# Kernel optimization log

Measured on AMD Instinct MI355X. Metric: run time of the kernel, lower is better.

Reference implementation:

```python
import jax, jax.numpy as jnp
import numpy as np

NEG = 1e12  # matches the torch code's -1e12 '-inf' substitute


def setup_inputs() -> dict:
    key = jax.random.key(0)
    k1, k2, k3, k4 = jax.random.split(key, 4)
    B, L, H, O = 8, 512, 768, 12
    inputs = jax.random.normal(k1, (B, L, H), dtype=jnp.float32)
    mask = jax.random.randint(k2, (B, L), 0, 2, dtype=jnp.int32)
    # kaiming-uniform-ish init scale
    bound1 = 1.0 / np.sqrt(H)
    weight1 = jax.random.uniform(k3, (H, O, H), dtype=jnp.float32, minval=-bound1, maxval=bound1)
    bound2 = 1.0 / np.sqrt(2 * H + 1)
    weight2 = jax.random.uniform(k4, (2 * H + 1, O), dtype=jnp.float32, minval=-bound2, maxval=bound2)
    return {"inputs": inputs, "weight1": weight1, "weight2": weight2, "mask": mask}


def reference(inputs, weight1, weight2, mask):
    B, L, H = inputs.shape
    # bilinear term: bxyo = x_i W1 x_j
    logits1 = jnp.einsum('bxi,ioj,byj->bxyo', inputs, weight1, inputs)
    # linear term: equivalent to cat([x_i, x_j, 1]) @ weight2, without the O(L^2*H) intermediate.
    # concat_x[b,i,j] = [inputs[b,i], inputs[b,j], 1]
    wa = weight2[:H]          # multiplies x_i (the x2/row side)
    wb = weight2[H:2 * H]     # multiplies x_j (the x1/col side)
    bias = weight2[2 * H]     # multiplies the ones column
    lin_i = inputs @ wa       # [B, L, O]
    lin_j = inputs @ wb       # [B, L, O]
    logits = logits1 + lin_i[:, :, None, :] + lin_j[:, None, :, :] + bias
    logits = jnp.transpose(logits, (0, 3, 1, 2))  # [B, O, L, L]
    m = mask.astype(logits.dtype)
    m_row = m[:, None, :, None]  # mask on axis ndim-2
    m_col = m[:, None, None, :]  # mask on axis ndim-1
    logits = logits * m_row - NEG * (1.0 - m_row)
    logits = logits * m_col - NEG * (1.0 - m_col)
    tril = jnp.tril(jnp.ones((L, L), logits.dtype), k=-1)
    logits = logits - tril * NEG
    return logits
```

## Files before the change

### kernel.cpp

```cpp
#include <hip/hip_runtime.h>


#define NEGV 1e12f

typedef __attribute__((ext_vector_type(4))) float f32x4;
typedef __attribute__((ext_vector_type(8))) int   i32x8;

__device__ __forceinline__ unsigned char f2fp8(float f) {
    union { float f; unsigned u; } c; c.f = f;
    unsigned s = (c.u >> 24) & 0x80;
    unsigned a = c.u & 0x7FFFFFFF;
    if (a < 0x3C800000u) return (unsigned char)s;
    a += 0x80000;
    int e = (int)(a >> 23) - 127;
    unsigned m = (a >> 20) & 7;
    if (e > 8 || (e == 8 && m == 7)) return (unsigned char)(s | 0x7E);
    return (unsigned char)(s | ((e + 7) << 3) | m);
}

__device__ __forceinline__ unsigned pk_fp8x2(float a, float b) {
#if __has_builtin(__builtin_amdgcn_cvt_pk_fp8_f32)
    return (unsigned)__builtin_amdgcn_cvt_pk_fp8_f32(a, b, 0, false) & 0xFFFFu;
#else
    return (unsigned)f2fp8(a) | ((unsigned)f2fp8(b) << 8);
#endif
}

__device__ __forceinline__ float fp8_to_f32(unsigned char b) {
#if __has_builtin(__builtin_amdgcn_cvt_f32_fp8)
    return __builtin_amdgcn_cvt_f32_fp8((int)b, 0);
#else
    const int s = b >> 7, e = (b >> 3) & 15, m = b & 7;
    float mag = e ? __builtin_ldexpf((float)(8 + m), e - 10)
                  : __builtin_ldexpf((float)m, -9);
    return s ? -mag : mag;
#endif
}

__device__ __forceinline__ unsigned f2fp4(float f) {
    const float a = fabsf(f);
    const unsigned s = (__float_as_uint(f) >> 28) & 8u;
    unsigned c;
    if      (a < 0.25f) c = 0;
    else if (a < 0.75f) c = 1;
    else if (a < 1.25f) c = 2;
    else if (a < 1.75f) c = 3;
    else if (a < 2.5f)  c = 4;
    else if (a < 3.5f)  c = 5;
    else if (a < 5.0f)  c = 6;
    else                c = 7;
    return s | c;
}

#define GLDS(gp, lp) __builtin_amdgcn_global_load_lds( \
    (__attribute__((address_space(1))) void*)(gp),     \
    (__attribute__((address_space(3))) void*)(lp), 16, 0, 0)

__global__ __launch_bounds__(256) void prep_kernel(
    const float* __restrict__ in, const float* __restrict__ w1,
    const float* __restrict__ w2, unsigned* __restrict__ A4,
    unsigned* __restrict__ A8, unsigned char* __restrict__ W4) {
    __shared__ float t[64][68];
    const int bx  = blockIdx.x;
    const int tid = threadIdx.x;
    if (bx < 1536) {
        const int i = bx * 256 + tid;
        const float4 v0 = ((const float4*)in)[2 * i];
        const float4 v1 = ((const float4*)in)[2 * i + 1];
        A4[i] = f2fp4(v0.x * 2.0f)        | (f2fp4(v0.y * 2.0f) << 4)
              | (f2fp4(v0.z * 2.0f) << 8) | (f2fp4(v0.w * 2.0f) << 12)
              | (f2fp4(v1.x * 2.0f) << 16)| (f2fp4(v1.y * 2.0f) << 20)
              | (f2fp4(v1.z * 2.0f) << 24)| (f2fp4(v1.w * 2.0f) << 28);
        A8[2 * i]     = pk_fp8x2(v0.x, v0.y) | (pk_fp8x2(v0.z, v0.w) << 16);
        A8[2 * i + 1] = pk_fp8x2(v1.x, v1.y) | (pk_fp8x2(v1.z, v1.w) << 16);
    } else if (bx < 3264) {
        const int b2 = bx - 1536;
        const int n0 = (b2 % 144) * 64;
        const int i0 = (b2 / 144) * 64;
        const int g  = tid >> 4;
        const int q  = tid & 15;
        #pragma unroll
        for (int p = 0; p < 4; ++p) {
            const int il = p * 16 + g;
            float4 v = *(const float4*)(w1 + (size_t)(i0 + il) * 9216 + n0 + q * 4);
            *(float4*)&t[il][q * 4] = v;
        }
        __syncthreads();
        #pragma unroll
        for (int p = 0; p < 2; ++p) {
            const int nl = p * 32 + (tid >> 3);
            const int iq = (tid & 7) * 8;
            unsigned w = 0;
            #pragma unroll
            for (int e = 0; e < 8; ++e)
                w |= f2fp4(t[iq + e][nl] * 128.0f) << (4 * e);
            *(unsigned*)(W4 + (size_t)(n0 + nl) * 384 + (i0 >> 1) + (tid & 7) * 4) = w;
        }
    } else {
        const int j = bx - 3264;
        unsigned char* dst = W4 + (size_t)(9216 + j) * 384;
        if (j < 24) {
            if (tid < 128) {
                const int h0 = tid * 6;
                #pragma unroll
                for (int k = 0; k < 3; ++k) {
                    const int h = h0 + 2 * k;
                    const int c0 = (j < 12) ? (h * 12 + j)       : ((768 + h) * 12 + (j - 12));
                    const int c1 = (j < 12) ? ((h + 1) * 12 + j) : ((769 + h) * 12 + (j - 12));
                    dst[(h >> 1)] = (unsigned char)(f2fp4(w2[c0] * 128.0f)
                                                  | (f2fp4(w2[c1] * 128.0f) << 4));
                }
            }
        } else {
            if (tid < 96) ((unsigned*)dst)[tid] = 0u;
        }
    }
}

__device__ __forceinline__ void gemm256_fp4(
    const unsigned char* __restrict__ A, int lda,
    const unsigned char* __restrict__ B, int ldb,
    char* As, char* Bs, f32x4 (&acc)[8][4], int sA, int sB) {
    const int tid  = threadIdx.x;
    const int lane = tid & 63;
    const int wave = tid >> 6;
    const unsigned char* aSrc[4]; const unsigned char* bSrc[4];
    int off[4];
    #pragma unroll
    for (int p = 0; p < 4; ++p) {
        const int cc = tid + 512 * p;
        const int row = cc >> 3, slot = cc & 7;
        const int g = slot ^ (row & 7);
        aSrc[p] = A + (size_t)row * lda + g * 16;
        bSrc[p] = B + (size_t)row * ldb + g * 16;
        off[p] = cc * 16;
    }
    const int wm = (wave >> 2) * 128;
    const int wn = (wave & 3) * 64;
    const int fr = lane & 15;
    const int kg = lane >> 4;

#define READ_FRAG4(dst, buf, rr, kk) do {                                         \
        const uint4 q_ = *(const uint4*)((buf) + (rr) * 128 +                     \
                                         (((kk) * 4 + kg) ^ ((rr) & 7)) * 16);    \
        dst[0] = q_.x; dst[1] = q_.y; dst[2] = q_.z; dst[3] = q_.w;               \
        dst[4] = 0; dst[5] = 0; dst[6] = 0; dst[7] = 0;                           \
    } while (0)

    #pragma unroll
    for (int p = 0; p < 4; ++p) GLDS(aSrc[p], As + off[p]);
    #pragma unroll
    for (int p = 0; p < 4; ++p) GLDS(bSrc[p], Bs + off[p]);
    __syncthreads();
    int cur = 0;
    #pragma unroll
    for (int t = 1; t <= 3; ++t) {
        const int nxt = cur ^ 1;
        if (t < 3) {
            const int kk = t * 128;
            #pragma unroll
            for (int p = 0; p < 4; ++p) GLDS(aSrc[p] + kk, As + nxt * 32768 + off[p]);
            #pragma unroll
            for (int p = 0; p < 4; ++p) GLDS(bSrc[p] + kk, Bs + nxt * 32768 + off[p]);
        }
        const char* Ab = As + cur * 32768;
        const char* Bb = Bs + cur * 32768;
        #pragma unroll
        for (int kk = 0; kk < 2; ++kk) {
            i32x8 bf[4];
            #pragma unroll
            for (int ni = 0; ni < 4; ++ni) READ_FRAG4(bf[ni], Bb, wn + ni * 16 + fr, kk);
            #pragma unroll
            for (int mi = 0; mi < 8; ++mi) {
                i32x8 af; READ_FRAG4(af, Ab, wm + mi * 16 + fr, kk);
                #pragma unroll
                for (int ni = 0; ni < 4; ++ni)
                    acc[mi][ni] = __builtin_amdgcn_mfma_scale_f32_16x16x128_f8f6f4(
                        af, bf[ni], acc[mi][ni], 4, 4, 0, sA, 0, sB);
            }
        }
        __syncthreads();
        cur = nxt;
    }
#undef READ_FRAG4
}

__device__ __forceinline__ void gemm256_fp8(
    const unsigned char* __restrict__ A, int lda,
    const unsigned char* __restrict__ B, int ldb,
    char* As, char* Bs, f32x4 (&acc)[8][4], int sA, int sB) {
    const int tid  = threadIdx.x;
    const int lane = tid & 63;
    const int wave = tid >> 6;
    const unsigned char* aSrc[4]; const unsigned char* bSrc[4];
    int off[4];
    #pragma unroll
    for (int p = 0; p < 4; ++p) {
        const int cc = tid + 512 * p;
        const int row = cc >> 3, slot = cc & 7;
        const int g = slot ^ (row & 7);
        aSrc[p] = A + (size_t)row * lda + g * 16;
        bSrc[p] = B + (size_t)row * ldb + g * 16;
        off[p] = cc * 16;
    }
    const int wm = (wave >> 2) * 128;
    const int wn = (wave & 3) * 64;
    const int fr = lane & 15;
    const int kg = lane >> 4;

    #pragma unroll
    for (int p = 0; p < 4; ++p) GLDS(aSrc[p], As + off[p]);
    #pragma unroll
    for (int p = 0; p < 4; ++p) GLDS(bSrc[p], Bs + off[p]);
    #pragma unroll
    for (int p = 0; p < 4; ++p) GLDS(aSrc[p] + 128, As + 32768 + off[p]);
    #pragma unroll
    for (int p = 0; p < 4; ++p) GLDS(bSrc[p] + 128, Bs + 32768 + off[p]);

    #pragma unroll
    for (int t = 0; t < 6; ++t) {
        const int cur = t & 1;
        if (t < 5) asm volatile("s_waitcnt vmcnt(8)" ::: "memory");
        else       asm volatile("s_waitcnt vmcnt(0)" ::: "memory");
        __builtin_amdgcn_sched_barrier(0);
        __builtin_amdgcn_s_barrier();
        const char* Ab = As + cur * 32768;
        const char* Bb = Bs + cur * 32768;
        i32x8 bf[4];
        #pragma unroll
        for (int ni = 0; ni < 4; ++ni) {
            const int r = wn + ni * 16 + fr;
            const uint4 lo = *(const uint4*)(Bb + r * 128 + ((2 * kg    ) ^ (r & 7)) * 16);
            const uint4 hi = *(const uint4*)(Bb + r * 128 + ((2 * kg + 1) ^ (r & 7)) * 16);
            bf[ni][0] = lo.x; bf[ni][1] = lo.y; bf[ni][2] = lo.z; bf[ni][3] = lo.w;
            bf[ni][4] = hi.x; bf[ni][5] = hi.y; bf[ni][6] = hi.z; bf[ni][7] = hi.w;
        }
        __builtin_amdgcn_s_setprio(1);
        #pragma unroll
        for (int mi = 0; mi < 8; ++mi) {
            const int r = wm + mi * 16 + fr;
            const uint4 lo = *(const uint4*)(Ab + r * 128 + ((2 * kg    ) ^ (r & 7)) * 16);
            const uint4 hi = *(const uint4*)(Ab + r * 128 + ((2 * kg + 1) ^ (r & 7)) * 16);
            i32x8 af;
            af[0] = lo.x; af[1] = lo.y; af[2] = lo.z; af[3] = lo.w;
            af[4] = hi.x; af[5] = hi.y; af[6] = hi.z; af[7] = hi.w;
            #pragma unroll
            for (int ni = 0; ni < 4; ++ni)
                acc[mi][ni] = __builtin_amdgcn_mfma_scale_f32_16x16x128_f8f6f4(
                    af, bf[ni], acc[mi][ni], 0, 0, 0, sA, 0, sB);
        }
        __builtin_amdgcn_s_setprio(0);
        asm volatile("s_waitcnt lgkmcnt(0)" ::: "memory");
        __builtin_amdgcn_sched_barrier(0);
        __builtin_amdgcn_s_barrier();
        if (t < 4) {
            const int kk = (t + 2) * 128;
            #pragma unroll
            for (int p = 0; p < 4; ++p) GLDS(aSrc[p] + kk, As + cur * 32768 + off[p]);
            #pragma unroll
            for (int p = 0; p < 4; ++p) GLDS(bSrc[p] + kk, Bs + cur * 32768 + off[p]);
        }
    }
}

__global__ __launch_bounds__(512, 2) void gemm1_kernel(
    const unsigned char* __restrict__ A4,
    const unsigned char* __restrict__ W4,
    unsigned char* __restrict__ U8) {
    __shared__ __align__(16) char As[2 * 32768];
    __shared__ __align__(16) char Bs[2 * 32768];
    const int orig = blockIdx.x;
    const int swz  = (orig & 7) * 74 + (orig >> 3);
    const int m0 = (swz & 15) * 256;
    const int n0 = (swz >> 4) * 256;
    f32x4 acc[8][4] = {};
    gemm256_fp4(A4 + (size_t)m0 * 384, 384, W4 + (size_t)n0 * 384, 384,
                As, Bs, acc, 0x7E7E7E7E, 0x78787878);
    const int lane = threadIdx.x & 63;
    const int wave = threadIdx.x >> 6;
    const int wm = (wave >> 2) * 128, wn = (wave & 3) * 64;
    const int rl = (lane >> 4) * 4, cl = lane & 15;
    #pragma unroll
    for (int mi = 0; mi < 8; ++mi) {
        const int m = m0 + wm + mi * 16 + rl;
        #pragma unroll
        for (int ni = 0; ni < 4; ++ni) {
            const int n = n0 + wn + ni * 16 + cl;
            const unsigned p01 = pk_fp8x2(acc[mi][ni][0], acc[mi][ni][1]);
            const unsigned p23 = pk_fp8x2(acc[mi][ni][2], acc[mi][ni][3]);
            U8[(size_t)(m    ) * 9472 + n] = (unsigned char)(p01 & 0xFF);
            U8[(size_t)(m + 1) * 9472 + n] = (unsigned char)(p01 >> 8);
            U8[(size_t)(m + 2) * 9472 + n] = (unsigned char)(p23 & 0xFF);
            U8[(size_t)(m + 3) * 9472 + n] = (unsigned char)(p23 >> 8);
        }
    }
}

__global__ __launch_bounds__(512, 2) void gemm2_kernel(
    const unsigned char* __restrict__ U8,
    const unsigned char* __restrict__ A8,
    const float* __restrict__ w2,
    const int* __restrict__ mask,
    float* __restrict__ out) {
    __shared__ __align__(16) char As[2 * 32768];
    __shared__ __align__(16) char Bs[2 * 32768];
    const int orig = blockIdx.x;
    const int swz  = (orig & 7) * 48 + (orig >> 3);
    const int bo = swz >> 2;
    const int b = bo / 12, o = bo % 12;
    const int x0 = (swz & 1) * 256;
    const int y0 = ((swz >> 1) & 1) * 256;
    f32x4 acc[8][4] = {};
    gemm256_fp8(U8 + (size_t)(b * 512 + x0) * 9472 + (size_t)o * 768, 9472,
                A8 + (size_t)(b * 512 + y0) * 768, 768,
                As, Bs, acc, 0x7F7F7F7F, 0x7F7F7F7F);
    const float bias = w2[1536 * 12 + o];
    float* outp = out + (size_t)bo * 512 * 512;
    const int lane = threadIdx.x & 63;
    const int wave = threadIdx.x >> 6;
    const int wm = (wave >> 2) * 128, wn = (wave & 3) * 64;
    const int rl = (lane >> 4) * 4, cl = lane & 15;
    float ljv[4]; int mc[4];
    #pragma unroll
    for (int ni = 0; ni < 4; ++ni) {
        const int y = y0 + wn + ni * 16 + cl;
        ljv[ni] = fp8_to_f32(U8[(size_t)(b * 512 + y) * 9472 + 9228 + o]);
        mc[ni]  = mask[b * 512 + y];
    }
    #pragma unroll
    for (int mi = 0; mi < 8; ++mi) {
        const int xb = x0 + wm + mi * 16 + rl;
        float liv[4]; int mr[4];
        #pragma unroll
        for (int r = 0; r < 4; ++r) {
            liv[r] = fp8_to_f32(U8[(size_t)(b * 512 + xb + r) * 9472 + 9216 + o]);
            mr[r]  = mask[b * 512 + xb + r];
        }
        #pragma unroll
        for (int ni = 0; ni < 4; ++ni) {
            const int y = y0 + wn + ni * 16 + cl;
            #pragma unroll
            for (int r = 0; r < 4; ++r) {
                float v = acc[mi][ni][r] + liv[r] + ljv[ni] + bias;
                if (!(mr[r] & mc[ni])) v = -NEGV;
                if (xb + r > y)        v -= NEGV;
                outp[(size_t)(xb + r) * 512 + y] = v;
            }
        }
    }
}

extern "C" void kernel_launch(void* const* d_in, const int* in_sizes, int n_in,
                              void* d_out, int out_size, void* d_ws, size_t ws_size,
                              hipStream_t stream) {
    const float* inputs = (const float*)d_in[0];
    const float* w1     = (const float*)d_in[1];
    const float* w2     = (const float*)d_in[2];
    const int*   mask   = (const int*)d_in[3];
    float* outp = (float*)d_out;

    char* ws = (char*)d_ws;
    unsigned char* A4 = (unsigned char*)(ws + 0);
    unsigned char* A8 = (unsigned char*)(ws + 1572864);
    unsigned char* W4 = (unsigned char*)(ws + 4718592);
    unsigned char* U8 = (unsigned char*)(ws + 8355840);

    prep_kernel<<<3520, 256, 0, stream>>>(inputs, w1, w2, (unsigned*)A4,
                                          (unsigned*)A8, W4);
    gemm1_kernel<<<592, 512, 0, stream>>>(A4, W4, U8);
    gemm2_kernel<<<384, 512, 0, stream>>>(U8, A8, w2, mask, outp);
}
```

Baseline: 204.0 us.

## Single-buffer LDS in fp4 GEMM to raise occupancy in gemm1

Replaces the double-buffered LDS pipeline in the fp4 GEMM with a single buffer that loads each k-tile, syncs, computes, then syncs again. This halves the shared memory per block (128KB to 64KB) and raises launch bounds to 4 blocks per CU, so other resident blocks are meant to hide load latency in place of in-block prefetch. The cost is no intra-block overlap of global loads with MFMA, plus tighter register pressure from the higher occupancy target, which may cause spills with 128 fp32 accumulators per thread.

```diff
diff --git a/kernel.cpp b/kernel.cpp
--- a/kernel.cpp
+++ b/kernel.cpp
@@ -117,7 +117,7 @@
     }
 }
 
-__device__ __forceinline__ void gemm256_fp4(
+__device__ __forceinline__ void gemm256_fp4_sb(
     const unsigned char* __restrict__ A, int lda,
     const unsigned char* __restrict__ B, int ldb,
     char* As, char* Bs, f32x4 (&acc)[8][4], int sA, int sB) {
@@ -148,31 +148,21 @@
     } while (0)
 
     #pragma unroll
-    for (int p = 0; p < 4; ++p) GLDS(aSrc[p], As + off[p]);
-    #pragma unroll
-    for (int p = 0; p < 4; ++p) GLDS(bSrc[p], Bs + off[p]);
-    __syncthreads();
-    int cur = 0;
-    #pragma unroll
-    for (int t = 1; t <= 3; ++t) {
-        const int nxt = cur ^ 1;
-        if (t < 3) {
-            const int kk = t * 128;
-            #pragma unroll
-            for (int p = 0; p < 4; ++p) GLDS(aSrc[p] + kk, As + nxt * 32768 + off[p]);
-            #pragma unroll
-            for (int p = 0; p < 4; ++p) GLDS(bSrc[p] + kk, Bs + nxt * 32768 + off[p]);
-        }
-        const char* Ab = As + cur * 32768;
-        const char* Bb = Bs + cur * 32768;
+    for (int t = 0; t < 3; ++t) {
+        const int kk0 = t * 128;
+        #pragma unroll
+        for (int p = 0; p < 4; ++p) GLDS(aSrc[p] + kk0, As + off[p]);
+        #pragma unroll
+        for (int p = 0; p < 4; ++p) GLDS(bSrc[p] + kk0, Bs + off[p]);
+        __syncthreads();
         #pragma unroll
         for (int kk = 0; kk < 2; ++kk) {
             i32x8 bf[4];
             #pragma unroll
-            for (int ni = 0; ni < 4; ++ni) READ_FRAG4(bf[ni], Bb, wn + ni * 16 + fr, kk);
+            for (int ni = 0; ni < 4; ++ni) READ_FRAG4(bf[ni], Bs, wn + ni * 16 + fr, kk);
             #pragma unroll
             for (int mi = 0; mi < 8; ++mi) {
-                i32x8 af; READ_FRAG4(af, Ab, wm + mi * 16 + fr, kk);
+                i32x8 af; READ_FRAG4(af, As, wm + mi * 16 + fr, kk);
                 #pragma unroll
                 for (int ni = 0; ni < 4; ++ni)
                     acc[mi][ni] = __builtin_amdgcn_mfma_scale_f32_16x16x128_f8f6f4(
@@ -180,7 +170,6 @@
             }
         }
         __syncthreads();
-        cur = nxt;
     }
 #undef READ_FRAG4
 }
@@ -263,19 +252,19 @@
     }
 }
 
-__global__ __launch_bounds__(512, 2) void gemm1_kernel(
+__global__ __launch_bounds__(512, 4) void gemm1_kernel(
     const unsigned char* __restrict__ A4,
     const unsigned char* __restrict__ W4,
     unsigned char* __restrict__ U8) {
-    __shared__ __align__(16) char As[2 * 32768];
-    __shared__ __align__(16) char Bs[2 * 32768];
+    __shared__ __align__(16) char As[32768];
+    __shared__ __align__(16) char Bs[32768];
     const int orig = blockIdx.x;
     const int swz  = (orig & 7) * 74 + (orig >> 3);
     const int m0 = (swz & 15) * 256;
     const int n0 = (swz >> 4) * 256;
     f32x4 acc[8][4] = {};
-    gemm256_fp4(A4 + (size_t)m0 * 384, 384, W4 + (size_t)n0 * 384, 384,
-                As, Bs, acc, 0x7E7E7E7E, 0x78787878);
+    gemm256_fp4_sb(A4 + (size_t)m0 * 384, 384, W4 + (size_t)n0 * 384, 384,
+                   As, Bs, acc, 0x7E7E7E7E, 0x78787878);
     const int lane = threadIdx.x & 63;
     const int wave = threadIdx.x >> 6;
     const int wm = (wave >> 2) * 128, wn = (wave & 3) * 64;
```

Result: slower. 316.1 us (+54.9%).
